# Optimization experiments

Hardware: AMD Instinct MI355X
Metric: run time of the kernel (lower is better)

Reference implementation:

```python
import jax, jax.numpy as jnp
import numpy as np
import math

MODEL_DIM = 4096
NUM_EXPERTS = 64
NUM_TOKENS = 8192
CAPACITY_FACTOR = 1.0
MIN_CAPACITY = 4


def setup_inputs() -> dict:
    key = jax.random.key(0)
    k1, k2, k3 = jax.random.split(key, 3)
    x = jax.random.normal(k1, (NUM_TOKENS, MODEL_DIM), dtype=jnp.float32)
    wg_weight = jax.random.normal(k2, (NUM_EXPERTS, MODEL_DIM), dtype=jnp.float32) * (1.0 / math.sqrt(MODEL_DIM))
    uniform_noise = jax.random.uniform(k3, (NUM_TOKENS, NUM_EXPERTS), dtype=jnp.float32)
    return {"x": x, "wg_weight": wg_weight, "uniform_noise": uniform_noise}


def reference(x, wg_weight, uniform_noise):
    # gate projection in fp32 (torch module forces .float())
    logits = jnp.einsum('sd,ed->se', x.astype(jnp.float32), wg_weight.astype(jnp.float32))
    gates = jax.nn.softmax(logits, axis=1)  # [s, e]
    s, e = gates.shape
    capacity = max(math.ceil(s / e * CAPACITY_FACTOR), MIN_CAPACITY)  # static: 128

    indices1_s = jnp.argmax(gates, axis=1)                      # [s]
    mask1 = jax.nn.one_hot(indices1_s, e, dtype=jnp.int32)      # [s, e]
    exp_counts = jnp.sum(mask1, axis=0)                         # [e]

    # load-balancing aux loss
    me = jnp.mean(gates, axis=0)
    ce = jnp.mean(mask1.astype(jnp.float32), axis=0)
    l_aux = jnp.sum(me * ce) * e

    # random capacity selection: per-expert top-`capacity` tokens by uniform noise
    mask1_rand = mask1.astype(jnp.float32) * uniform_noise      # [s, e]
    _, top_idx = jax.lax.top_k(mask1_rand.T, capacity)          # [e, capacity] token ids
    sel = jnp.zeros((s, e), jnp.int32).at[top_idx, jnp.arange(e)[:, None]].set(1)
    new_mask1 = mask1 * sel                                     # [s, e]

    # capacity-slot assignment via cumsum
    locations1 = jnp.cumsum(new_mask1, axis=0) - 1              # [s, e]
    locations1_s = jnp.sum(locations1 * new_mask1, axis=1)      # [s]

    gates_masked = gates * new_mask1.astype(jnp.float32)        # [s, e]
    locations1_sc = jax.nn.one_hot(locations1_s, capacity, dtype=jnp.float32)  # [s, c]
    combine_weights = jnp.einsum('se,sc->sec', gates_masked, locations1_sc)     # [s, e, c]
    dispatch_mask = combine_weights.astype(bool)
    return l_aux, combine_weights, dispatch_mask, exp_counts
```

## Files before the change

kernel.cpp:

```cpp
#include <hip/hip_runtime.h>

#define S    8192
#define Dm   4096
#define E    64
#define CAP  128
#define CCH  16
#define KC   (Dm/CCH)
#define TBv  256
#define KSUB 64
#define XS_STRIDE 65

#define CW_OFF 1
#define DM_OFF (1 + (size_t)S*E*CAP)
#define EC_OFF (1 + 2*(size_t)S*E*CAP)

__global__ void k0_transpose(const float* __restrict__ wg, float* __restrict__ wt) {
    const int e  = blockIdx.x >> 2;
    const int kb = (blockIdx.x & 3) * 1024;
    const int t  = threadIdx.x;
    const float4 v = *(const float4*)(wg + (size_t)e * Dm + kb + t * 4);
    wt[(size_t)(kb + t*4 + 0) * E + e] = v.x;
    wt[(size_t)(kb + t*4 + 1) * E + e] = v.y;
    wt[(size_t)(kb + t*4 + 2) * E + e] = v.z;
    wt[(size_t)(kb + t*4 + 3) * E + e] = v.w;
}

__global__ __launch_bounds__(256, 2)
void k1_partial(const float* __restrict__ x, const float* __restrict__ wt,
                float* __restrict__ part) {
    __shared__ float xs[TBv * XS_STRIDE];
    const int tb  = blockIdx.x >> 4;
    const int c   = blockIdx.x & 15;
    const int tid = threadIdx.x;
    const int token = tb * TBv + tid;
    const int k0 = c * KC;

    float acc[E];
    #pragma unroll
    for (int e = 0; e < E; e++) acc[e] = 0.f;

    for (int su = 0; su < KC / KSUB; su++) {
        const int ks0 = k0 + su * KSUB;
        {
            const int r0 = tid >> 4;
            const int c4 = tid & 15;
            #pragma unroll
            for (int i = 0; i < 16; i++) {
                const int row = i * 16 + r0;
                const float4 v = *(const float4*)(x + (size_t)(tb*TBv + row) * Dm + ks0 + c4*4);
                float* p = xs + row * XS_STRIDE + c4 * 4;
                p[0] = v.x; p[1] = v.y; p[2] = v.z; p[3] = v.w;
            }
        }
        __syncthreads();
        const float* wrow = wt + (size_t)ks0 * E;
        #pragma unroll 4
        for (int kk = 0; kk < KSUB; kk++) {
            const float xv = xs[tid * XS_STRIDE + kk];
            const float* wr = wrow + kk * E;
            #pragma unroll
            for (int e = 0; e < E; e++) acc[e] = fmaf(xv, wr[e], acc[e]);
        }
        __syncthreads();
    }
    float* dst = part + ((size_t)c * S + token) * E;
    #pragma unroll
    for (int e = 0; e < E; e += 4) {
        *(float4*)(dst + e) = make_float4(acc[e], acc[e+1], acc[e+2], acc[e+3]);
    }
}

__global__ __launch_bounds__(256, 1)
void k1b_softmax(const float* __restrict__ part, float* __restrict__ gate_val,
                 int* __restrict__ idx1, int* __restrict__ counts,
                 float* __restrict__ me_sum) {
    const int tid = threadIdx.x, wv = tid >> 6, ln = tid & 63;
    const int token = blockIdx.x * 4 + wv;
    float p = 0.f;
    #pragma unroll
    for (int c = 0; c < CCH; c++) p += part[((size_t)c * S + token) * E + ln];
    float v = p; int i = ln;
    #pragma unroll
    for (int off = 1; off < 64; off <<= 1) {
        float ov = __shfl_xor(v, off, 64);
        int   oi = __shfl_xor(i, off, 64);
        if (ov > v || (ov == v && oi < i)) { v = ov; i = oi; }
    }
    float g = __expf(p - v);
    float ssum = g;
    #pragma unroll
    for (int off = 1; off < 64; off <<= 1) ssum += __shfl_xor(ssum, off, 64);
    const float gate = g / ssum;
    __shared__ float gs[4][64];
    gs[wv][ln] = gate;
    __syncthreads();
    if (tid < 64)
        atomicAdd(&me_sum[tid], gs[0][tid] + gs[1][tid] + gs[2][tid] + gs[3][tid]);
    if (ln == 0) {
        gate_val[token] = 1.0f / ssum;
        idx1[token] = i;
        atomicAdd(&counts[i], 1);
    }
}

__device__ __forceinline__ int block_reduce_sum(int v, int* tmp4, int tid) {
    #pragma unroll
    for (int off = 1; off < 64; off <<= 1) v += __shfl_xor(v, off, 64);
    __syncthreads();
    if ((tid & 63) == 0) tmp4[tid >> 6] = v;
    __syncthreads();
    return tmp4[0] + tmp4[1] + tmp4[2] + tmp4[3];
}

__device__ __forceinline__ int block_scan_incl(int val, int* a, int* b, int tid, int* total) {
    __syncthreads();
    a[tid] = val;
    __syncthreads();
    int* src = a; int* dst = b;
    #pragma unroll
    for (int off = 1; off < 256; off <<= 1) {
        int v = src[tid];
        if (tid >= off) v += src[tid - off];
        dst[tid] = v;
        __syncthreads();
        int* t = src; src = dst; dst = t;
    }
    *total = src[255];
    return src[tid];
}

__global__ __launch_bounds__(256, 1)
void k2_select(const int* __restrict__ idx1, const float* __restrict__ gate_val,
               const float* __restrict__ noise, const int* __restrict__ counts,
               const float* __restrict__ me_sum, float* __restrict__ out) {
    const int e = blockIdx.x;
    const int tid = threadIdx.x;
    __shared__ int idx_s[S];
    __shared__ unsigned short l_tok[S];
    __shared__ float l_ns[S];
    __shared__ int sa[256], sb[256];
    __shared__ int tmp4[4];

    for (int i = tid; i < S; i += 256) idx_s[i] = idx1[i];
    __syncthreads();

    int cnt = 0;
    #pragma unroll
    for (int j4 = 0; j4 < 8; j4++) {
        const int4 q = *(const int4*)&idx_s[tid * 32 + j4 * 4];
        cnt += (q.x == e) + (q.y == e) + (q.z == e) + (q.w == e);
    }
    int total_n;
    int incl = block_scan_incl(cnt, sa, sb, tid, &total_n);
    int pos = incl - cnt;
    const int n = total_n;
    #pragma unroll
    for (int j4 = 0; j4 < 8; j4++) {
        const int4 q = *(const int4*)&idx_s[tid * 32 + j4 * 4];
        const int qv[4] = {q.x, q.y, q.z, q.w};
        #pragma unroll
        for (int u = 0; u < 4; u++) {
            const int s = tid * 32 + j4 * 4 + u;
            if (qv[u] == e) {
                l_tok[pos] = (unsigned short)s;
                l_ns[pos]  = noise[(size_t)s * E + e];
                pos++;
            }
        }
    }
    __syncthreads();

    if (tid == 0) out[EC_OFF + e] = (float)n;

    unsigned int V = 0u;
    if (n > CAP) {
        unsigned int lo = 0u, hi = 0x3F800000u;
        while (hi - lo > 1u) {
            const unsigned int mid = (lo + hi) >> 1;
            int c = 0;
            for (int i2 = tid; i2 < n; i2 += 256)
                c += (__float_as_uint(l_ns[i2]) >= mid);
            const int cge = block_reduce_sum(c, tmp4, tid);
            if (cge >= CAP) lo = mid; else hi = mid;
        }
        V = lo;
    }

    const int m = (n + 255) >> 8;
    const int i_begin = min(n, tid * m);
    const int i_end   = min(n, i_begin + m);
    int gt_l = 0, eq_l = 0;
    for (int i2 = i_begin; i2 < i_end; i2++) {
        const unsigned int b = __float_as_uint(l_ns[i2]);
        gt_l += (b > V); eq_l += (b == V);
    }
    int tot_gt, tot_eq;
    const int incl_gt = block_scan_incl(gt_l, sa, sb, tid, &tot_gt);
    (void)incl_gt;
    const int incl_eq = block_scan_incl(eq_l, sa, sb, tid, &tot_eq);
    const int eq_excl = incl_eq - eq_l;
    const int take_eq = CAP - tot_gt;
    const int sel_l = gt_l + max(0, min(eq_l, take_eq - eq_excl));
    int tot_sel;
    const int incl_sel = block_scan_incl(sel_l, sa, sb, tid, &tot_sel);
    int slot = incl_sel - sel_l;
    int eq_seen = eq_excl;
    for (int i2 = i_begin; i2 < i_end; i2++) {
        const unsigned int b = __float_as_uint(l_ns[i2]);
        bool sel;
        if (b > V) sel = true;
        else if (b == V) { sel = (eq_seen < take_eq); eq_seen++; }
        else sel = false;
        if (sel) {
            const int tok = l_tok[i2];
            const float g = gate_val[tok];
            const size_t off = (size_t)tok * (E * CAP) + (size_t)e * CAP + slot;
            out[CW_OFF + off] = g;
            out[DM_OFF + off] = 1.0f;
            slot++;
        }
    }

    if (e == 0 && tid < 64) {
        float la = (me_sum[tid] / (float)S) * ((float)counts[tid] / (float)S);
        #pragma unroll
        for (int off = 1; off < 64; off <<= 1) la += __shfl_xor(la, off, 64);
        if (tid == 0) out[0] = la * (float)E;
    }
}

extern "C" void kernel_launch(void* const* d_in, const int* in_sizes, int n_in,
                              void* d_out, int out_size, void* d_ws, size_t ws_size,
                              hipStream_t stream) {
    const float* x     = (const float*)d_in[0];
    const float* wg    = (const float*)d_in[1];
    const float* noise = (const float*)d_in[2];
    float* out = (float*)d_out;
    float* ws  = (float*)d_ws;

    float* gate_val = ws;
    int*   idx1     = (int*)(ws + 8192);
    int*   counts   = (int*)(ws + 16384);
    float* me_sum   = ws + 16448;

    float* dm_base = out + DM_OFF;
    float* wt      = dm_base;
    float* part    = dm_base + (size_t)Dm * E;

    hipMemsetAsync(counts, 0, 128 * sizeof(int), stream);
    k0_transpose<<<dim3(256), dim3(256), 0, stream>>>(wg, wt);
    k1_partial  <<<dim3(512), dim3(256), 0, stream>>>(x, wt, part);
    k1b_softmax <<<dim3(S/4), dim3(256), 0, stream>>>(part, gate_val, idx1, counts, me_sum);
    hipMemsetAsync(out, 0, (size_t)out_size * sizeof(float), stream);
    k2_select   <<<dim3(E),   dim3(256), 0, stream>>>(idx1, gate_val, noise, counts, me_sum, out);
}
```

Baseline: 790.8 us.

## Fuse gate GEMM with softmax/argmax and repack weights for lane-per-expert access

Replaces the split-K GEMM with partial-sum buffers plus a separate softmax kernel by one fused kernel. In it each wave covers a quarter of the K dimension for 16 tokens, with one lane per expert, and the waves reduce through shared memory before doing softmax/argmax in place. Weights are repacked into float4-interleaved rows, and the workspace is used instead of borrowing the output buffer. This removes the large partial-sum write/read and one kernel launch. In exchange, x is read as per-lane broadcast float4 loads with no LDS staging, and the per-block grid changes.

```diff
diff --git a/kernel.cpp b/kernel.cpp
--- a/kernel.cpp
+++ b/kernel.cpp
@@ -4,103 +4,85 @@
 #define Dm   4096
 #define E    64
 #define CAP  128
-#define CCH  16
-#define KC   (Dm/CCH)
-#define TBv  256
-#define KSUB 64
-#define XS_STRIDE 65
 
 #define CW_OFF 1
 #define DM_OFF (1 + (size_t)S*E*CAP)
 #define EC_OFF (1 + 2*(size_t)S*E*CAP)
 
-__global__ void k0_transpose(const float* __restrict__ wg, float* __restrict__ wt) {
-    const int e  = blockIdx.x >> 2;
-    const int kb = (blockIdx.x & 3) * 1024;
-    const int t  = threadIdx.x;
-    const float4 v = *(const float4*)(wg + (size_t)e * Dm + kb + t * 4);
-    wt[(size_t)(kb + t*4 + 0) * E + e] = v.x;
-    wt[(size_t)(kb + t*4 + 1) * E + e] = v.y;
-    wt[(size_t)(kb + t*4 + 2) * E + e] = v.z;
-    wt[(size_t)(kb + t*4 + 3) * E + e] = v.w;
+__global__ void k0_pack(const float* __restrict__ wg, float* __restrict__ wt2) {
+    const int g  = blockIdx.x * 256 + threadIdx.x;
+    const int e  = g & 63;
+    const int k4 = g >> 6;
+    const float4 v = *(const float4*)(wg + (size_t)e * Dm + k4 * 4);
+    *(float4*)(wt2 + (size_t)k4 * 256 + e * 4) = v;
 }
 
 __global__ __launch_bounds__(256, 2)
-void k1_partial(const float* __restrict__ x, const float* __restrict__ wt,
-                float* __restrict__ part) {
-    __shared__ float xs[TBv * XS_STRIDE];
-    const int tb  = blockIdx.x >> 4;
-    const int c   = blockIdx.x & 15;
-    const int tid = threadIdx.x;
-    const int token = tb * TBv + tid;
-    const int k0 = c * KC;
-
-    float acc[E];
-    #pragma unroll
-    for (int e = 0; e < E; e++) acc[e] = 0.f;
-
-    for (int su = 0; su < KC / KSUB; su++) {
-        const int ks0 = k0 + su * KSUB;
-        {
-            const int r0 = tid >> 4;
-            const int c4 = tid & 15;
-            #pragma unroll
-            for (int i = 0; i < 16; i++) {
-                const int row = i * 16 + r0;
-                const float4 v = *(const float4*)(x + (size_t)(tb*TBv + row) * Dm + ks0 + c4*4);
-                float* p = xs + row * XS_STRIDE + c4 * 4;
-                p[0] = v.x; p[1] = v.y; p[2] = v.z; p[3] = v.w;
-            }
-        }
-        __syncthreads();
-        const float* wrow = wt + (size_t)ks0 * E;
-        #pragma unroll 4
-        for (int kk = 0; kk < KSUB; kk++) {
-            const float xv = xs[tid * XS_STRIDE + kk];
-            const float* wr = wrow + kk * E;
-            #pragma unroll
-            for (int e = 0; e < E; e++) acc[e] = fmaf(xv, wr[e], acc[e]);
-        }
-        __syncthreads();
-    }
-    float* dst = part + ((size_t)c * S + token) * E;
-    #pragma unroll
-    for (int e = 0; e < E; e += 4) {
-        *(float4*)(dst + e) = make_float4(acc[e], acc[e+1], acc[e+2], acc[e+3]);
-    }
-}
-
-__global__ __launch_bounds__(256, 1)
-void k1b_softmax(const float* __restrict__ part, float* __restrict__ gate_val,
-                 int* __restrict__ idx1, int* __restrict__ counts,
-                 float* __restrict__ me_sum) {
-    const int tid = threadIdx.x, wv = tid >> 6, ln = tid & 63;
-    const int token = blockIdx.x * 4 + wv;
-    float p = 0.f;
-    #pragma unroll
-    for (int c = 0; c < CCH; c++) p += part[((size_t)c * S + token) * E + ln];
-    float v = p; int i = ln;
-    #pragma unroll
-    for (int off = 1; off < 64; off <<= 1) {
-        float ov = __shfl_xor(v, off, 64);
-        int   oi = __shfl_xor(i, off, 64);
-        if (ov > v || (ov == v && oi < i)) { v = ov; i = oi; }
-    }
-    float g = __expf(p - v);
-    float ssum = g;
-    #pragma unroll
-    for (int off = 1; off < 64; off <<= 1) ssum += __shfl_xor(ssum, off, 64);
-    const float gate = g / ssum;
-    __shared__ float gs[4][64];
-    gs[wv][ln] = gate;
-    __syncthreads();
-    if (tid < 64)
-        atomicAdd(&me_sum[tid], gs[0][tid] + gs[1][tid] + gs[2][tid] + gs[3][tid]);
-    if (ln == 0) {
-        gate_val[token] = 1.0f / ssum;
-        idx1[token] = i;
-        atomicAdd(&counts[i], 1);
-    }
+void k1_fused(const float* __restrict__ x, const float* __restrict__ wt2,
+              float* __restrict__ gate_val, int* __restrict__ idx1,
+              int* __restrict__ counts, float* __restrict__ me_sum) {
+    __shared__ float red[4 * 16 * 64];
+    const int tid  = threadIdx.x;
+    const int lane = tid & 63;
+    const int wv   = __builtin_amdgcn_readfirstlane(tid >> 6);
+    const int tok0 = blockIdx.x * 16;
+
+    const float* xp = x   + ((size_t)tok0 << 12) + ((size_t)wv << 10);
+    const float* wp = wt2 + ((size_t)wv << 16) + (lane << 2);
+
+    float acc[16];
+    #pragma unroll
+    for (int t = 0; t < 16; t++) acc[t] = 0.f;
+
+    float4 w4 = *(const float4*)(wp);
+    for (int k = 0; k < 1024; k += 4) {
+        const float4 w4n = *(const float4*)(wp + 256);
+        #pragma unroll
+        for (int t = 0; t < 16; t++) {
+            const float4 xv = *(const float4*)(xp + (size_t)t * Dm + k);
+            acc[t] = fmaf(xv.x, w4.x, acc[t]);
+            acc[t] = fmaf(xv.y, w4.y, acc[t]);
+            acc[t] = fmaf(xv.z, w4.z, acc[t]);
+            acc[t] = fmaf(xv.w, w4.w, acc[t]);
+        }
+        w4 = w4n;
+        wp += 256;
+    }
+
+    #pragma unroll
+    for (int t = 0; t < 16; t++) red[(wv * 16 + t) * 64 + lane] = acc[t];
+    __syncthreads();
+
+    float meg = 0.f;
+    #pragma unroll
+    for (int j = 0; j < 4; j++) {
+        const int tt = j * 4 + wv;
+        float p = red[(0 * 16 + tt) * 64 + lane] + red[(1 * 16 + tt) * 64 + lane]
+                + red[(2 * 16 + tt) * 64 + lane] + red[(3 * 16 + tt) * 64 + lane];
+        float v = p; int im = lane;
+        #pragma unroll
+        for (int off = 1; off < 64; off <<= 1) {
+            float ov = __shfl_xor(v, off, 64);
+            int   oi = __shfl_xor(im, off, 64);
+            if (ov > v || (ov == v && oi < im)) { v = ov; im = oi; }
+        }
+        float g = __expf(p - v);
+        float ssum = g;
+        #pragma unroll
+        for (int off = 1; off < 64; off <<= 1) ssum += __shfl_xor(ssum, off, 64);
+        meg += g / ssum;
+        if (lane == 0) {
+            gate_val[tok0 + tt] = 1.0f / ssum;
+            idx1[tok0 + tt] = im;
+            atomicAdd(&counts[im], 1);
+        }
+    }
+    __syncthreads();
+    red[wv * 64 + lane] = meg;
+    __syncthreads();
+    if (wv == 0)
+        atomicAdd(&me_sum[lane],
+                  red[lane] + red[64 + lane] + red[128 + lane] + red[192 + lane]);
 }
 
 __device__ __forceinline__ int block_reduce_sum(int v, int* tmp4, int tid) {
@@ -242,15 +224,11 @@
     int*   idx1     = (int*)(ws + 8192);
     int*   counts   = (int*)(ws + 16384);
     float* me_sum   = ws + 16448;
-
-    float* dm_base = out + DM_OFF;
-    float* wt      = dm_base;
-    float* part    = dm_base + (size_t)Dm * E;
+    float* wt2      = ws + 16512;
 
     hipMemsetAsync(counts, 0, 128 * sizeof(int), stream);
-    k0_transpose<<<dim3(256), dim3(256), 0, stream>>>(wg, wt);
-    k1_partial  <<<dim3(512), dim3(256), 0, stream>>>(x, wt, part);
-    k1b_softmax <<<dim3(S/4), dim3(256), 0, stream>>>(part, gate_val, idx1, counts, me_sum);
     hipMemsetAsync(out, 0, (size_t)out_size * sizeof(float), stream);
-    k2_select   <<<dim3(E),   dim3(256), 0, stream>>>(idx1, gate_val, noise, counts, me_sum, out);
-}
+    k0_pack <<<dim3(256),  dim3(256), 0, stream>>>(wg, wt2);
+    k1_fused<<<dim3(S/16), dim3(256), 0, stream>>>(x, wt2, gate_val, idx1, counts, me_sum);
+    k2_select<<<dim3(E),   dim3(256), 0, stream>>>(idx1, gate_val, noise, counts, me_sum, out);
+}
```

Measured after the change: 928.5 us. +17.4%, slower.

## Register-block two tokens per thread and stage gate weights in LDS

Applied to the files above, without the earlier changes.

The gate-projection kernel now has each thread accumulate two tokens against all 64 experts. The weight sub-tile is staged in shared memory as float4 instead of being read from global memory inside the inner loop, and the K split is doubled to 32 chunks with 512-token tiles. This aims to raise FMA-per-load reuse and cut global weight traffic. The transposed weights and partial sums move from the output buffer into the workspace, and the output memset is issued first. The costs are a larger partial-sum buffer for the softmax kernel to reduce, and higher register and LDS pressure.

```diff
diff --git a/kernel.cpp b/kernel.cpp
--- a/kernel.cpp
+++ b/kernel.cpp
@@ -4,69 +4,91 @@
 #define Dm   4096
 #define E    64
 #define CAP  128
-#define CCH  16
+#define CCH  32
 #define KC   (Dm/CCH)
-#define TBv  256
-#define KSUB 64
-#define XS_STRIDE 65
+#define TBv  512
+#define KSUB 32
+#define XSTR 33
 
 #define CW_OFF 1
 #define DM_OFF (1 + (size_t)S*E*CAP)
 #define EC_OFF (1 + 2*(size_t)S*E*CAP)
 
-__global__ void k0_transpose(const float* __restrict__ wg, float* __restrict__ wt) {
+__global__ void k0_transpose(const float* __restrict__ wg, float* __restrict__ wt2) {
     const int e  = blockIdx.x >> 2;
     const int kb = (blockIdx.x & 3) * 1024;
     const int t  = threadIdx.x;
     const float4 v = *(const float4*)(wg + (size_t)e * Dm + kb + t * 4);
-    wt[(size_t)(kb + t*4 + 0) * E + e] = v.x;
-    wt[(size_t)(kb + t*4 + 1) * E + e] = v.y;
-    wt[(size_t)(kb + t*4 + 2) * E + e] = v.z;
-    wt[(size_t)(kb + t*4 + 3) * E + e] = v.w;
+    wt2[(size_t)(kb + t*4 + 0) * E + e] = v.x;
+    wt2[(size_t)(kb + t*4 + 1) * E + e] = v.y;
+    wt2[(size_t)(kb + t*4 + 2) * E + e] = v.z;
+    wt2[(size_t)(kb + t*4 + 3) * E + e] = v.w;
 }
 
 __global__ __launch_bounds__(256, 2)
-void k1_partial(const float* __restrict__ x, const float* __restrict__ wt,
+void k1_partial(const float* __restrict__ x, const float* __restrict__ wt2,
                 float* __restrict__ part) {
-    __shared__ float xs[TBv * XS_STRIDE];
-    const int tb  = blockIdx.x >> 4;
-    const int c   = blockIdx.x & 15;
+    __shared__ float  xs[TBv * XSTR];
+    __shared__ float4 ws4[KSUB * 16];
+    const int tb  = blockIdx.x >> 5;
+    const int c   = blockIdx.x & 31;
     const int tid = threadIdx.x;
-    const int token = tb * TBv + tid;
+    const int lane = tid & 63;
+    const int wv   = tid >> 6;
     const int k0 = c * KC;
 
-    float acc[E];
-    #pragma unroll
-    for (int e = 0; e < E; e++) acc[e] = 0.f;
+    const int ta = wv * 128 + lane;
+    const int xa_base = ta * XSTR;
+    const int xb_base = xa_base + 64 * XSTR;
+
+    float acca[64], accb[64];
+    #pragma unroll
+    for (int e = 0; e < 64; e++) { acca[e] = 0.f; accb[e] = 0.f; }
+
+    const int r0 = tid >> 3;
+    const int c4 = tid & 7;
 
     for (int su = 0; su < KC / KSUB; su++) {
         const int ks0 = k0 + su * KSUB;
+        #pragma unroll
+        for (int i = 0; i < 16; i++) {
+            const int row = i * 32 + r0;
+            const float4 v = *(const float4*)(x + (size_t)(tb*TBv + row) * Dm + ks0 + c4*4);
+            float* p = xs + row * XSTR + c4 * 4;
+            p[0] = v.x; p[1] = v.y; p[2] = v.z; p[3] = v.w;
+        }
         {
-            const int r0 = tid >> 4;
-            const int c4 = tid & 15;
+            const float* wsrc = wt2 + (size_t)ks0 * E;
+            ws4[tid]       = *(const float4*)(wsrc + tid * 4);
+            ws4[tid + 256] = *(const float4*)(wsrc + 1024 + tid * 4);
+        }
+        __syncthreads();
+        #pragma unroll 2
+        for (int kk = 0; kk < KSUB; kk++) {
+            const float xa = xs[xa_base + kk];
+            const float xb = xs[xb_base + kk];
             #pragma unroll
-            for (int i = 0; i < 16; i++) {
-                const int row = i * 16 + r0;
-                const float4 v = *(const float4*)(x + (size_t)(tb*TBv + row) * Dm + ks0 + c4*4);
-                float* p = xs + row * XS_STRIDE + c4 * 4;
-                p[0] = v.x; p[1] = v.y; p[2] = v.z; p[3] = v.w;
+            for (int e4 = 0; e4 < 16; e4++) {
+                const float4 w = ws4[kk * 16 + e4];
+                acca[e4*4+0] = fmaf(xa, w.x, acca[e4*4+0]);
+                acca[e4*4+1] = fmaf(xa, w.y, acca[e4*4+1]);
+                acca[e4*4+2] = fmaf(xa, w.z, acca[e4*4+2]);
+                acca[e4*4+3] = fmaf(xa, w.w, acca[e4*4+3]);
+                accb[e4*4+0] = fmaf(xb, w.x, accb[e4*4+0]);
+                accb[e4*4+1] = fmaf(xb, w.y, accb[e4*4+1]);
+                accb[e4*4+2] = fmaf(xb, w.z, accb[e4*4+2]);
+                accb[e4*4+3] = fmaf(xb, w.w, accb[e4*4+3]);
             }
         }
         __syncthreads();
-        const float* wrow = wt + (size_t)ks0 * E;
-        #pragma unroll 4
-        for (int kk = 0; kk < KSUB; kk++) {
-            const float xv = xs[tid * XS_STRIDE + kk];
-            const float* wr = wrow + kk * E;
-            #pragma unroll
-            for (int e = 0; e < E; e++) acc[e] = fmaf(xv, wr[e], acc[e]);
-        }
-        __syncthreads();
-    }
-    float* dst = part + ((size_t)c * S + token) * E;
-    #pragma unroll
-    for (int e = 0; e < E; e += 4) {
-        *(float4*)(dst + e) = make_float4(acc[e], acc[e+1], acc[e+2], acc[e+3]);
+    }
+    const size_t tok_a = (size_t)tb * TBv + ta;
+    float* pa = part + ((size_t)c * S + tok_a) * E;
+    float* pb = pa + 64 * E;
+    #pragma unroll
+    for (int e4 = 0; e4 < 16; e4++) {
+        *(float4*)(pa + e4*4) = make_float4(acca[e4*4], acca[e4*4+1], acca[e4*4+2], acca[e4*4+3]);
+        *(float4*)(pb + e4*4) = make_float4(accb[e4*4], accb[e4*4+1], accb[e4*4+2], accb[e4*4+3]);
     }
 }
 
@@ -242,15 +264,13 @@
     int*   idx1     = (int*)(ws + 8192);
     int*   counts   = (int*)(ws + 16384);
     float* me_sum   = ws + 16448;
-
-    float* dm_base = out + DM_OFF;
-    float* wt      = dm_base;
-    float* part    = dm_base + (size_t)Dm * E;
+    float* wt2      = ws + 16512;
+    float* part     = ws + 16512 + 262144;
 
     hipMemsetAsync(counts, 0, 128 * sizeof(int), stream);
-    k0_transpose<<<dim3(256), dim3(256), 0, stream>>>(wg, wt);
-    k1_partial  <<<dim3(512), dim3(256), 0, stream>>>(x, wt, part);
-    k1b_softmax <<<dim3(S/4), dim3(256), 0, stream>>>(part, gate_val, idx1, counts, me_sum);
     hipMemsetAsync(out, 0, (size_t)out_size * sizeof(float), stream);
-    k2_select   <<<dim3(E),   dim3(256), 0, stream>>>(idx1, gate_val, noise, counts, me_sum, out);
-}
+    k0_transpose<<<dim3(256),  dim3(256), 0, stream>>>(wg, wt2);
+    k1_partial  <<<dim3(512),  dim3(256), 0, stream>>>(x, wt2, part);
+    k1b_softmax <<<dim3(S/4),  dim3(256), 0, stream>>>(part, gate_val, idx1, counts, me_sum);
+    k2_select   <<<dim3(E),    dim3(256), 0, stream>>>(idx1, gate_val, noise, counts, me_sum, out);
+}
```

New measurement: 798.9 us. About the same (+1.0%).

## Register-tile gate GEMM with shared-memory weight staging and drop transpose kernel

Applied to the files above, without the earlier changes.

The gate projection kernel now computes an 8x8 token-by-expert register tile per thread. Both x and the weight slice are staged in shared memory as K-major tiles, replacing the old scheme where each thread computed one token against all 64 experts, reading weights from global memory. The separate weight-transpose kernel is removed, and partial sums move to workspace, so the output memset can be issued up front. The K dimension is split into 32 chunks, which gives 1024 blocks and doubles the partial-sum traffic that the softmax kernel must reduce.

```diff
diff --git a/kernel.cpp b/kernel.cpp
--- a/kernel.cpp
+++ b/kernel.cpp
@@ -4,69 +4,75 @@
 #define Dm   4096
 #define E    64
 #define CAP  128
-#define CCH  16
+#define CCH  32
 #define KC   (Dm/CCH)
-#define TBv  256
-#define KSUB 64
-#define XS_STRIDE 65
+#define KSUB 16
+#define XSTR 260
+#define WSTR 68
 
 #define CW_OFF 1
 #define DM_OFF (1 + (size_t)S*E*CAP)
 #define EC_OFF (1 + 2*(size_t)S*E*CAP)
 
-__global__ void k0_transpose(const float* __restrict__ wg, float* __restrict__ wt) {
-    const int e  = blockIdx.x >> 2;
-    const int kb = (blockIdx.x & 3) * 1024;
-    const int t  = threadIdx.x;
-    const float4 v = *(const float4*)(wg + (size_t)e * Dm + kb + t * 4);
-    wt[(size_t)(kb + t*4 + 0) * E + e] = v.x;
-    wt[(size_t)(kb + t*4 + 1) * E + e] = v.y;
-    wt[(size_t)(kb + t*4 + 2) * E + e] = v.z;
-    wt[(size_t)(kb + t*4 + 3) * E + e] = v.w;
-}
-
-__global__ __launch_bounds__(256, 2)
-void k1_partial(const float* __restrict__ x, const float* __restrict__ wt,
+__global__ __launch_bounds__(256, 4)
+void k1_partial(const float* __restrict__ x, const float* __restrict__ wg,
                 float* __restrict__ part) {
-    __shared__ float xs[TBv * XS_STRIDE];
-    const int tb  = blockIdx.x >> 4;
-    const int c   = blockIdx.x & 15;
+    __shared__ float xs[KSUB][XSTR];
+    __shared__ float ws[KSUB][WSTR];
+    const int tb  = blockIdx.x >> 5;
+    const int c   = blockIdx.x & 31;
     const int tid = threadIdx.x;
-    const int token = tb * TBv + tid;
-    const int k0 = c * KC;
-
-    float acc[E];
-    #pragma unroll
-    for (int e = 0; e < E; e++) acc[e] = 0.f;
+    const int tt  = tid & 31;
+    const int ee  = tid >> 5;
+    const int k0  = c * KC;
+
+    float acc[64];
+    #pragma unroll
+    for (int i = 0; i < 64; i++) acc[i] = 0.f;
+
+    const int xr = tid >> 2;
+    const int xc = tid & 3;
+    const int we = tid >> 2;
+    const int wk = (tid & 3) * 4;
 
     for (int su = 0; su < KC / KSUB; su++) {
         const int ks0 = k0 + su * KSUB;
+        #pragma unroll
+        for (int i = 0; i < 4; i++) {
+            const int row = i * 64 + xr;
+            const float4 v = *(const float4*)(x + (size_t)(tb*256 + row) * Dm + ks0 + xc*4);
+            xs[xc*4+0][row] = v.x;
+            xs[xc*4+1][row] = v.y;
+            xs[xc*4+2][row] = v.z;
+            xs[xc*4+3][row] = v.w;
+        }
         {
-            const int r0 = tid >> 4;
-            const int c4 = tid & 15;
-            #pragma unroll
-            for (int i = 0; i < 16; i++) {
-                const int row = i * 16 + r0;
-                const float4 v = *(const float4*)(x + (size_t)(tb*TBv + row) * Dm + ks0 + c4*4);
-                float* p = xs + row * XS_STRIDE + c4 * 4;
-                p[0] = v.x; p[1] = v.y; p[2] = v.z; p[3] = v.w;
-            }
+            const float4 v = *(const float4*)(wg + (size_t)we * Dm + ks0 + wk);
+            ws[wk+0][we] = v.x; ws[wk+1][we] = v.y;
+            ws[wk+2][we] = v.z; ws[wk+3][we] = v.w;
         }
         __syncthreads();
-        const float* wrow = wt + (size_t)ks0 * E;
         #pragma unroll 4
         for (int kk = 0; kk < KSUB; kk++) {
-            const float xv = xs[tid * XS_STRIDE + kk];
-            const float* wr = wrow + kk * E;
+            const float4 a0 = *(const float4*)&xs[kk][tt*8];
+            const float4 a1 = *(const float4*)&xs[kk][tt*8+4];
+            const float4 w0 = *(const float4*)&ws[kk][ee*8];
+            const float4 w1 = *(const float4*)&ws[kk][ee*8+4];
+            const float av[8] = {a0.x,a0.y,a0.z,a0.w,a1.x,a1.y,a1.z,a1.w};
+            const float wv[8] = {w0.x,w0.y,w0.z,w0.w,w1.x,w1.y,w1.z,w1.w};
             #pragma unroll
-            for (int e = 0; e < E; e++) acc[e] = fmaf(xv, wr[e], acc[e]);
+            for (int t = 0; t < 8; t++)
+                #pragma unroll
+                for (int e = 0; e < 8; e++)
+                    acc[t*8+e] = fmaf(av[t], wv[e], acc[t*8+e]);
         }
         __syncthreads();
     }
-    float* dst = part + ((size_t)c * S + token) * E;
-    #pragma unroll
-    for (int e = 0; e < E; e += 4) {
-        *(float4*)(dst + e) = make_float4(acc[e], acc[e+1], acc[e+2], acc[e+3]);
+    #pragma unroll
+    for (int t = 0; t < 8; t++) {
+        float* dst = part + ((size_t)c * S + tb*256 + tt*8 + t) * E + ee*8;
+        *(float4*)(dst)     = make_float4(acc[t*8+0], acc[t*8+1], acc[t*8+2], acc[t*8+3]);
+        *(float4*)(dst + 4) = make_float4(acc[t*8+4], acc[t*8+5], acc[t*8+6], acc[t*8+7]);
     }
 }
 
@@ -242,15 +248,11 @@
     int*   idx1     = (int*)(ws + 8192);
     int*   counts   = (int*)(ws + 16384);
     float* me_sum   = ws + 16448;
-
-    float* dm_base = out + DM_OFF;
-    float* wt      = dm_base;
-    float* part    = dm_base + (size_t)Dm * E;
+    float* part     = ws + 16512;
 
     hipMemsetAsync(counts, 0, 128 * sizeof(int), stream);
-    k0_transpose<<<dim3(256), dim3(256), 0, stream>>>(wg, wt);
-    k1_partial  <<<dim3(512), dim3(256), 0, stream>>>(x, wt, part);
-    k1b_softmax <<<dim3(S/4), dim3(256), 0, stream>>>(part, gate_val, idx1, counts, me_sum);
     hipMemsetAsync(out, 0, (size_t)out_size * sizeof(float), stream);
-    k2_select   <<<dim3(E),   dim3(256), 0, stream>>>(idx1, gate_val, noise, counts, me_sum, out);
-}
+    k1_partial  <<<dim3(1024), dim3(256), 0, stream>>>(x, wg, part);
+    k1b_softmax <<<dim3(S/4),  dim3(256), 0, stream>>>(part, gate_val, idx1, counts, me_sum);
+    k2_select   <<<dim3(E),    dim3(256), 0, stream>>>(idx1, gate_val, noise, counts, me_sum, out);
+}
```

Measured after the change: 715.5 us. 9.5% less time.
